# Optimization experiments

Hardware: AMD Instinct MI355X
Metric: run time of the kernel (lower is better)

The kernel has to match this reference:

```python
import jax, jax.numpy as jnp
import numpy as np

B, D, SL, N, H, LL = 2, 128, 1024, 64, 4, 4
LN_EPS = 1e-5
DIST_EPS = 1e-8


def _ln(x, g, b):
    m = x.mean(-1, keepdims=True)
    v = ((x - m) ** 2).mean(-1, keepdims=True)
    return (x - m) / jnp.sqrt(v + LN_EPS) * g + b


def _sla(x, qw, qb, kw, kb, vw, vb, ow, ob):
    # x: [B, R, C, D]; rank-1 scaled linear attention (head_qk_dim = 1)
    Bq, R, C, Dd = x.shape
    Hh = qw.shape[0]
    hd = Dd // Hh
    q = jnp.einsum('brcd,hd->brhc', x, qw) + qb[:, None]   # [B,R,H,C]
    k = jnp.einsum('brcd,hd->brhc', x, kw) + kb[:, None]
    q = jax.nn.elu(q) + 1.0
    k = jax.nn.elu(k) + 1.0
    q = q / q.mean(-1, keepdims=True)
    k = k / k.sum(-1, keepdims=True)
    v = (jnp.einsum('brcd,ed->brce', x, vw) + vb).reshape(Bq, R, C, Hh, hd)
    v = v.transpose(0, 1, 3, 2, 4)                         # [B,R,H,C,hd]
    ktv = jnp.einsum('brhc,brhce->brhe', k, v)             # [B,R,H,hd]
    V = jnp.einsum('brhc,brhe->brche', q, ktv)             # [B,R,C,H,hd]
    V = V.reshape(Bq, R, C, Dd)
    return jnp.einsum('brcd,ed->brce', V, ow) + ob


def _forward(x, rq_w, rq_b, rk_w, rk_b, rv_w, rv_b, ro_w, ro_b,
             cq_w, cq_b, ck_w, ck_b, cv_w, cv_b, co_w, co_b,
             ln_r_g, ln_r_b, ln_c_g, ln_c_b, ln_f_g, ln_f_b,
             f1_w, f1_b, f2_w, f2_b):
    y = x.transpose(0, 2, 3, 1)   # [B, L, N, D] channels-last

    def layer(y, p):
        (rqw, rqb, rkw, rkb, rvw, rvb, row_, rob,
         cqw, cqb, ckw, ckb, cvw, cvb, cow, cob,
         lrg, lrb, lcg, lcb, lfg, lfb, f1w, f1b, f2w, f2b) = p
        # row attention: rows = L, cols = N
        y = y + _sla(_ln(y, lrg, lrb), rqw, rqb, rkw, rkb, rvw, rvb, row_, rob)
        # col attention: rows = N, cols = L
        hc = _ln(y, lcg, lcb).swapaxes(1, 2)
        y = y + _sla(hc, cqw, cqb, ckw, ckb, cvw, cvb, cow, cob).swapaxes(1, 2)
        # FFN (1x1 convs == pointwise linears)
        hf = _ln(y, lfg, lfb)
        hf = jax.nn.gelu(jnp.einsum('blnd,ed->blne', hf, f1w) + f1b, approximate=False)
        y = y + (jnp.einsum('blne,de->blnd', hf, f2w) + f2b)
        return y, None

    params = (rq_w, rq_b, rk_w, rk_b, rv_w, rv_b, ro_w, ro_b,
              cq_w, cq_b, ck_w, ck_b, cv_w, cv_b, co_w, co_b,
              ln_r_g, ln_r_b, ln_c_g, ln_c_b, ln_f_g, ln_f_b,
              f1_w, f1_b, f2_w, f2_b)
    y, _ = jax.lax.scan(layer, y, params)

    # Euclidean pairwise distance head (use_cls=False): mean over sites 1..L
    xb = y[:, 1:].mean(axis=1)                 # [B, N, D]
    i0, i1 = np.tril_indices(N, -1)            # lower=True, diff=True ordering
    diffs = xb[:, i0] - xb[:, i1]              # [B, n_pairs, D]
    return jnp.sqrt(jnp.sum(diffs * diffs, axis=-1) + DIST_EPS)


def setup_inputs() -> dict:
    key = jax.random.key(0)
    ks = jax.random.split(key, 12)
    s = 0.02
    z = lambda *sh: jnp.zeros(sh, jnp.float32)
    o = lambda *sh: jnp.ones(sh, jnp.float32)
    w = lambda k, sh: jax.random.normal(k, sh, jnp.float32) * s
    p = {'x': jax.random.normal(ks[0], (B, D, SL, N), jnp.float32)}
    p['rq_w'] = w(ks[1], (LL, H, D)); p['rq_b'] = z(LL, H)
    p['rk_w'] = w(ks[2], (LL, H, D)); p['rk_b'] = z(LL, H)
    p['rv_w'] = w(ks[3], (LL, D, D)); p['rv_b'] = z(LL, D)
    p['ro_w'] = w(ks[4], (LL, D, D)); p['ro_b'] = z(LL, D)
    p['cq_w'] = w(ks[5], (LL, H, D)); p['cq_b'] = z(LL, H)
    p['ck_w'] = w(ks[6], (LL, H, D)); p['ck_b'] = z(LL, H)
    p['cv_w'] = w(ks[7], (LL, D, D)); p['cv_b'] = z(LL, D)
    p['co_w'] = w(ks[8], (LL, D, D)); p['co_b'] = z(LL, D)
    p['ln_r_g'] = o(LL, D); p['ln_r_b'] = z(LL, D)
    p['ln_c_g'] = o(LL, D); p['ln_c_b'] = z(LL, D)
    p['ln_f_g'] = o(LL, D); p['ln_f_b'] = z(LL, D)
    p['f1_w'] = w(ks[9], (LL, 4 * D, D)); p['f1_b'] = z(LL, 4 * D)
    p['f2_w'] = w(ks[10], (LL, D, 4 * D)); p['f2_b'] = z(LL, D)
    return p


def reference(x, rq_w, rq_b, rk_w, rk_b, rv_w, rv_b, ro_w, ro_b,
              cq_w, cq_b, ck_w, ck_b, cv_w, cv_b, co_w, co_b,
              ln_r_g, ln_r_b, ln_c_g, ln_c_b, ln_f_g, ln_f_b,
              f1_w, f1_b, f2_w, f2_b):
    return _forward(x, rq_w, rq_b, rk_w, rk_b, rv_w, rv_b, ro_w, ro_b,
                    cq_w, cq_b, ck_w, ck_b, cv_w, cv_b, co_w, co_b,
                    ln_r_g, ln_r_b, ln_c_g, ln_c_b, ln_f_g, ln_f_b,
                    f1_w, f1_b, f2_w, f2_b)
```

## Files before the change

### kernel.cpp

```cpp
#include <hip/hip_runtime.h>
#include <math.h>

#define LCNT 4

typedef float f32x4 __attribute__((ext_vector_type(4)));
typedef short bf16x8 __attribute__((ext_vector_type(8)));
typedef unsigned int u32;

__device__ __forceinline__ ushort bfr(float x){
  unsigned int b = __float_as_uint(x);
  return (ushort)((b + 0x7FFFu + ((b>>16)&1u)) >> 16);
}
__device__ __forceinline__ unsigned int pk2(float a, float b){
  return (unsigned int)bfr(a) | ((unsigned int)bfr(b)<<16);
}
__device__ __forceinline__ float bflo(u32 u){ return __uint_as_float(u<<16); }
__device__ __forceinline__ float bfhi(u32 u){ return __uint_as_float(u & 0xffff0000u); }
__device__ __forceinline__ float fast_gelu(float v){
  float v2 = v*v;
  float u = v*(-1.5957691f - 0.0713548162f*v2);
  float e = __expf(u);
  return v*__builtin_amdgcn_rcpf(1.f + e);
}
__device__ __forceinline__ void gl_lds16(const void* g, void* l){
  __builtin_amdgcn_global_load_lds(
      (const __attribute__((address_space(1))) u32*)g,
      (__attribute__((address_space(3))) u32*)l, 16, 0, 0);
}

__global__ __launch_bounds__(256) void k_transpose(const float* __restrict__ x,
                                                   float* __restrict__ y){
  int g = blockIdx.x;
  int b = g >> 10, l = g & 1023;
  __shared__ float sh[128*65];
  for (int idx = threadIdx.x; idx < 128*64; idx += 256){
    int d = idx >> 6, n = idx & 63;
    sh[d*65+n] = x[(((size_t)b*128 + d)*1024 + l)*64 + n];
  }
  __syncthreads();
  for (int idx = threadIdx.x; idx < 128*64; idx += 256){
    int n = idx >> 7, d = idx & 127;
    y[((size_t)g*64 + n)*128 + d] = sh[d*65+n];
  }
}

__global__ __launch_bounds__(256) void k_cvt(const float* __restrict__ src,
                                             ushort* __restrict__ dst, int n4){
  int i = blockIdx.x*256 + threadIdx.x;
  if (i < n4){
    float4 v = ((const float4*)src)[i];
    ushort4 p; p.x=bfr(v.x); p.y=bfr(v.y); p.z=bfr(v.z); p.w=bfr(v.w);
    ((ushort4*)dst)[i] = p;
  }
}

#define HSTRB 136
__global__ __launch_bounds__(256) void k_row(
    float* __restrict__ y,
    const float* __restrict__ rqw, const float* __restrict__ rqb,
    const float* __restrict__ rkw, const float* __restrict__ rkb,
    const float* __restrict__ rvw, const float* __restrict__ rvb,
    const float* __restrict__ roW, const float* __restrict__ rob,
    const float* __restrict__ lrg, const float* __restrict__ lrb,
    const float* __restrict__ cqw, const float* __restrict__ cqb,
    const float* __restrict__ ckw, const float* __restrict__ ckb,
    const float* __restrict__ lcg, const float* __restrict__ lcb,
    float2* __restrict__ stats,
    float* __restrict__ qout, float* __restrict__ kout)
{
  int g = blockIdx.x;
  __shared__ __align__(16) ushort sh_h[64*HSTRB];
  __shared__ __align__(16) float sh_w4[2048];
  __shared__ float sh_q[256], sh_k[256];
  __shared__ __align__(16) float sh_hkP[512];
  __shared__ __align__(16) float sh_ktv[128];
  int tid = threadIdx.x;
  int wid = tid>>6, ln = tid&63;

  {
    const float* wsrc = (wid==0)?rqw:(wid==1)?rkw:(wid==2)?cqw:ckw;
    gl_lds16(wsrc + ln*4,       &sh_w4[wid*512]);
    gl_lds16(wsrc + 256 + ln*4, &sh_w4[wid*512 + 256]);
  }

  int ttk = tid>>2, s4 = tid&3;
  float* yr = y + ((size_t)g*64 + ttk)*128 + s4*32;
  float4 v[8];
  #pragma unroll
  for (int i=0;i<8;i++) v[i] = *(const float4*)(yr + i*4);
  float sum = 0.f;
  #pragma unroll
  for (int i=0;i<8;i++) sum += v[i].x+v[i].y+v[i].z+v[i].w;
  sum += __shfl_xor(sum,1); sum += __shfl_xor(sum,2);
  float mean = sum*(1.0f/128.0f);
  float vs = 0.f;
  #pragma unroll
  for (int i=0;i<8;i++){
    v[i].x-=mean; v[i].y-=mean; v[i].z-=mean; v[i].w-=mean;
    vs += v[i].x*v[i].x+v[i].y*v[i].y+v[i].z*v[i].z+v[i].w*v[i].w;
  }
  vs += __shfl_xor(vs,1); vs += __shfl_xor(vs,2);
  float rstd = rsqrtf(vs*(1.0f/128.0f) + 1e-5f);
  {
    const float* gp = lrg + s4*32; const float* bp = lrb + s4*32;
    ushort* hrow = &sh_h[ttk*HSTRB + s4*32];
    #pragma unroll
    for (int i=0;i<8;i++){
      float4 g4 = *(const float4*)(gp+i*4);
      float4 b4 = *(const float4*)(bp+i*4);
      uint2 o2;
      o2.x = pk2(v[i].x*rstd*g4.x+b4.x, v[i].y*rstd*g4.y+b4.y);
      o2.y = pk2(v[i].z*rstd*g4.z+b4.z, v[i].w*rstd*g4.w+b4.w);
      *(uint2*)&hrow[i*4] = o2;
    }
  }
  __syncthreads();

  int h = tid>>6, n = tid&63;
  {
    float qr = rqb[h], kr = rkb[h];
    const int4* hp = (const int4*)&sh_h[n*HSTRB];
    const float4* qwp = (const float4*)&sh_w4[h*128];
    const float4* kwp = (const float4*)&sh_w4[512 + h*128];
    #pragma unroll 4
    for (int j=0;j<16;j++){
      int4 h8 = hp[j];
      float4 qa = qwp[2*j], qb4 = qwp[2*j+1];
      float4 ka = kwp[2*j], kb4 = kwp[2*j+1];
      float h0=bflo((u32)h8.x), h1=bfhi((u32)h8.x);
      float h2=bflo((u32)h8.y), h3=bfhi((u32)h8.y);
      float h4=bflo((u32)h8.z), h5=bfhi((u32)h8.z);
      float h6=bflo((u32)h8.w), h7=bfhi((u32)h8.w);
      qr += h0*qa.x+h1*qa.y+h2*qa.z+h3*qa.w + h4*qb4.x+h5*qb4.y+h6*qb4.z+h7*qb4.w;
      kr += h0*ka.x+h1*ka.y+h2*ka.z+h3*ka.w + h4*kb4.x+h5*kb4.y+h6*kb4.z+h7*kb4.w;
    }
    qr = qr > 0.f ? qr + 1.f : __expf(qr);
    kr = kr > 0.f ? kr + 1.f : __expf(kr);
    float qs = qr; for (int m=32;m>=1;m>>=1) qs += __shfl_xor(qs, m);
    float ks = kr; for (int m=32;m>=1;m>>=1) ks += __shfl_xor(ks, m);
    sh_q[h*64+n] = qr * (64.f/qs);
    sh_k[h*64+n] = kr * (1.f/ks);
  }
  __syncthreads();
  #pragma unroll
  for (int r=0;r<2;r++){
    int idx = tid + r*256;
    int hh = idx>>7, d = idx&127;
    float acc = 0.f;
    #pragma unroll 4
    for (int nn=0;nn<64;nn++)
      acc += sh_k[hh*64+nn]*bflo((u32)sh_h[nn*HSTRB+d]);
    sh_hkP[hh*128+d] = acc;
  }
  __syncthreads();
  if (tid < 128){
    float acc = rvb[tid];
    const float4* vr = (const float4*)(rvw + (size_t)tid*128);
    const float4* hp2 = (const float4*)(sh_hkP + (tid>>5)*128);
    #pragma unroll 8
    for (int j=0;j<32;j++){
      float4 a = vr[j], bq = hp2[j];
      acc += a.x*bq.x + a.y*bq.y + a.z*bq.z + a.w*bq.w;
    }
    sh_ktv[tid] = acc;
  }
  __syncthreads();
  #pragma unroll
  for (int r=0;r<2;r++){
    int idx = tid + r*256;
    int hh = idx>>7, e = idx&127;
    float acc = 0.f;
    const float4* orow = (const float4*)(roW + (size_t)e*128 + hh*32);
    const float4* kt = (const float4*)(sh_ktv + hh*32);
    #pragma unroll
    for (int j=0;j<8;j++){
      float4 a = orow[j], bq = kt[j];
      acc += a.x*bq.x + a.y*bq.y + a.z*bq.z + a.w*bq.w;
    }
    sh_hkP[hh*128+e] = acc;
  }
  __syncthreads();
  {
    float q0=sh_q[ttk], q1=sh_q[64+ttk], q2=sh_q[128+ttk], q3=sh_q[192+ttk];
    const float4* P4 = (const float4*)sh_hkP;
    #pragma unroll
    for (int i=0;i<8;i++){
      int d4 = s4*8 + i;
      float4 p0=P4[d4], p1=P4[32+d4], p2=P4[64+d4], p3=P4[96+d4];
      float4 o4=*(const float4*)&rob[s4*32+i*4];
      v[i].x += mean + o4.x + q0*p0.x+q1*p1.x+q2*p2.x+q3*p3.x;
      v[i].y += mean + o4.y + q0*p0.y+q1*p1.y+q2*p2.y+q3*p3.y;
      v[i].z += mean + o4.z + q0*p0.z+q1*p1.z+q2*p2.z+q3*p3.z;
      v[i].w += mean + o4.w + q0*p0.w+q1*p1.w+q2*p2.w+q3*p3.w;
      *(float4*)(yr + i*4) = v[i];
    }
  }
  float sum2 = 0.f;
  #pragma unroll
  for (int i=0;i<8;i++) sum2 += v[i].x+v[i].y+v[i].z+v[i].w;
  sum2 += __shfl_xor(sum2,1); sum2 += __shfl_xor(sum2,2);
  float cmean = sum2*(1.0f/128.0f);
  float cvs = 0.f;
  #pragma unroll
  for (int i=0;i<8;i++){
    v[i].x-=cmean; v[i].y-=cmean; v[i].z-=cmean; v[i].w-=cmean;
    cvs += v[i].x*v[i].x+v[i].y*v[i].y+v[i].z*v[i].z+v[i].w*v[i].w;
  }
  cvs += __shfl_xor(cvs,1); cvs += __shfl_xor(cvs,2);
  float crstd = rsqrtf(cvs*(1.0f/128.0f) + 1e-5f);
  if (s4 == 0) stats[(size_t)g*64 + ttk] = make_float2(cmean, crstd);
  {
    const float* gp = lcg + s4*32; const float* bp = lcb + s4*32;
    ushort* hrow = &sh_h[ttk*HSTRB + s4*32];
    #pragma unroll
    for (int i=0;i<8;i++){
      float4 g4 = *(const float4*)(gp+i*4);
      float4 b4 = *(const float4*)(bp+i*4);
      uint2 o2;
      o2.x = pk2(v[i].x*crstd*g4.x+b4.x, v[i].y*crstd*g4.y+b4.y);
      o2.y = pk2(v[i].z*crstd*g4.z+b4.z, v[i].w*crstd*g4.w+b4.w);
      *(uint2*)&hrow[i*4] = o2;
    }
  }
  __syncthreads();
  {
    float qv = cqb[h], kv = ckb[h];
    const int4* hp = (const int4*)&sh_h[n*HSTRB];
    const float4* qwp = (const float4*)&sh_w4[1024 + h*128];
    const float4* kwp = (const float4*)&sh_w4[1536 + h*128];
    #pragma unroll 4
    for (int j=0;j<16;j++){
      int4 h8 = hp[j];
      float4 qa = qwp[2*j], qb4 = qwp[2*j+1];
      float4 ka = kwp[2*j], kb4 = kwp[2*j+1];
      float h0=bflo((u32)h8.x), h1=bfhi((u32)h8.x);
      float h2=bflo((u32)h8.y), h3=bfhi((u32)h8.y);
      float h4=bflo((u32)h8.z), h5=bfhi((u32)h8.z);
      float h6=bflo((u32)h8.w), h7=bfhi((u32)h8.w);
      qv += h0*qa.x+h1*qa.y+h2*qa.z+h3*qa.w + h4*qb4.x+h5*qb4.y+h6*qb4.z+h7*qb4.w;
      kv += h0*ka.x+h1*ka.y+h2*ka.z+h3*ka.w + h4*kb4.x+h5*kb4.y+h6*kb4.z+h7*kb4.w;
    }
    qv = qv > 0.f ? qv + 1.f : __expf(qv);
    kv = kv > 0.f ? kv + 1.f : __expf(kv);
    size_t o = (size_t)g*256 + tid;
    qout[o] = qv; kout[o] = kv;
  }
}

__global__ __launch_bounds__(256) void k_qsum(const float* __restrict__ qin,
                                              float* __restrict__ qsp){
  int gg = blockIdx.x;
  int c = gg&7, b = gg>>3;
  int tid = threadIdx.x;
  const float* qp = qin + ((size_t)b*1024 + c*128)*256 + tid;
  float s = 0.f;
  #pragma unroll 4
  for (int j=0;j<128;j++){ s += *qp; qp += 256; }
  qsp[(size_t)gg*256 + tid] = s;
}

__global__ __launch_bounds__(256) void k_col_s1(
    const float* __restrict__ y, const float2* __restrict__ stats,
    const float* __restrict__ kin,
    float* __restrict__ s1p, float* __restrict__ Ab, float* __restrict__ Bb)
{
  int gg = blockIdx.x;
  int s = gg & 7, n = (gg>>3) & 63, b = gg>>9;
  int tid = threadIdx.x;
  int li = tid>>7, d = tid&127;
  const float* kp = kin + (size_t)b*262144 + n;
  float a0=0.f,a1=0.f,a2=0.f,a3=0.f;
  float A0=0.f,A1=0.f,A2=0.f,A3=0.f;
  float B0=0.f,B1=0.f,B2=0.f,B3=0.f;
  for (int j=0;j<64;j++){
    int l = s*128 + 2*j + li;
    size_t t = ((size_t)(b*1024+l)*64+n);
    float2 st = stats[t];
    float w = st.y * y[t*128 + d];
    float rm = st.y*st.x;
    const float* kl = kp + (size_t)l*256;
    float k0 = kl[0], k1 = kl[64], k2 = kl[128], k3 = kl[192];
    a0 += k0*w; a1 += k1*w; a2 += k2*w; a3 += k3*w;
    A0 += k0; A1 += k1; A2 += k2; A3 += k3;
    B0 += k0*rm; B1 += k1*rm; B2 += k2*rm; B3 += k3*rm;
  }
  __shared__ float shr[512];
  __shared__ float sAB[8];
  if (li == 1){
    shr[0*128+d]=a0; shr[1*128+d]=a1; shr[2*128+d]=a2; shr[3*128+d]=a3;
    if (d==0){ sAB[0]=A0; sAB[1]=A1; sAB[2]=A2; sAB[3]=A3;
               sAB[4]=B0; sAB[5]=B1; sAB[6]=B2; sAB[7]=B3; }
  }
  __syncthreads();
  if (li == 0){
    float* out = s1p + (size_t)gg*512;
    out[0*128+d] = a0 + shr[0*128+d];
    out[1*128+d] = a1 + shr[1*128+d];
    out[2*128+d] = a2 + shr[2*128+d];
    out[3*128+d] = a3 + shr[3*128+d];
    if (d==0){
      Ab[gg*4+0]=A0+sAB[0]; Ab[gg*4+1]=A1+sAB[1];
      Ab[gg*4+2]=A2+sAB[2]; Ab[gg*4+3]=A3+sAB[3];
      Bb[gg*4+0]=B0+sAB[4]; Bb[gg*4+1]=B1+sAB[5];
      Bb[gg*4+2]=B2+sAB[6]; Bb[gg*4+3]=B3+sAB[7];
    }
  }
}

__global__ __launch_bounds__(256) void k_col_ktvP(
    const float* __restrict__ s1p,
    const float* __restrict__ Ab, const float* __restrict__ Bb,
    const float* __restrict__ qsp,
    const float* __restrict__ vw, const float* __restrict__ vb,
    const float* __restrict__ ow,
    const float* __restrict__ lcg, const float* __restrict__ lcb,
    float* __restrict__ Pout)
{
  int gg = blockIdx.x;
  int b = gg>>6, n = gg&63;
  __shared__ float sh_hk[512];
  __shared__ float sh_ktv[128];
  __shared__ float sh_A[4], sh_B[4], sh_qs[4];
  int tid = threadIdx.x;
  #pragma unroll
  for (int r = 0; r < 2; r++){
    int idx = tid + r*256;
    float acc = 0.f;
    #pragma unroll
    for (int s = 0; s < 8; s++) acc += s1p[((size_t)gg*8 + s)*512 + idx];
    sh_hk[idx] = acc;
  }
  if (tid < 4){
    float a=0.f, bb=0.f, q=0.f;
    #pragma unroll
    for (int s = 0; s < 8; s++){ a += Ab[(gg*8+s)*4+tid]; bb += Bb[(gg*8+s)*4+tid]; }
    #pragma unroll
    for (int c = 0; c < 8; c++) q += qsp[((b*8+c)<<8) + (tid<<6) + n];
    sh_A[tid]=a; sh_B[tid]=bb; sh_qs[tid] = 1024.f/q;
  }
  __syncthreads();
  #pragma unroll
  for (int r = 0; r < 2; r++){
    int idx = tid + r*256;
    int h = idx>>7, d = idx&127;
    sh_hk[idx] = lcg[d]*((sh_hk[idx]-sh_B[h])/sh_A[h]) + lcb[d];
  }
  __syncthreads();
  if (tid < 128){
    float acc = vb[tid];
    const float* vr = vw + (size_t)tid*128;
    const float* hp2 = sh_hk + (tid>>5)*128;
    #pragma unroll 4
    for (int d = 0; d < 128; d++) acc += vr[d]*hp2[d];
    sh_ktv[tid] = acc;
  }
  __syncthreads();
  #pragma unroll
  for (int r = 0; r < 2; r++){
    int idx = tid + r*256;
    int hh = idx >> 7, e = idx & 127;
    float acc = 0.f;
    const float* orow = ow + (size_t)e*128 + hh*32;
    #pragma unroll 4
    for (int j = 0; j < 32; j++) acc += orow[j]*sh_ktv[hh*32+j];
    Pout[(size_t)gg*512 + hh*128 + e] = acc * sh_qs[hh];
  }
}

__global__ __launch_bounds__(512, 4) void k_ffn(
    float* __restrict__ y,
    const float* __restrict__ qbuf, const float* __restrict__ Pb,
    const float* __restrict__ cob,
    const float* __restrict__ gam, const float* __restrict__ bet,
    const ushort* __restrict__ w1b, const float* __restrict__ b1,
    const ushort* __restrict__ w2b, const float* __restrict__ b2)
{
  __shared__ __align__(16) ushort pool[29952];
  ushort* sW1 = pool;
  ushort* sW2 = pool + 8192;
  ushort* sH  = pool + 16384;
  ushort* sHf = pool + 25088;
  float*  sF  = (float*)pool;
  int tid = threadIdx.x;
  int g = blockIdx.x;
  size_t tb = (size_t)g*64;

  int wid = tid>>6, ln = tid&63;
  int lr = ln&15, gq = ln>>4;
  int wt = wid>>1, we = wid&1;
  int t0 = wt*16;

  #pragma unroll
  for (int i = 0; i < 2; i++){
    int row = wid*8 + i*4 + (ln>>4);
    gl_lds16(w1b + (size_t)row*128 + (((ln&15) ^ (row&7))<<3),
             &sW1[(wid*8 + i*4)*128]);
  }
  #pragma unroll
  for (int i = 0; i < 2; i++){
    int row = wid*16 + i*8 + (ln>>3);
    gl_lds16(w2b + (size_t)row*512 + (((ln&7) ^ (row&7))<<3),
             &sW2[(wid*16 + i*8)*64]);
  }

  int ttk = tid>>3, s8 = tid&7;
  float* yr = y + (tb+ttk)*128 + s8*16;
  float4 v[4];
  float fmean;
  {
    #pragma unroll
    for (int i = 0; i < 4; i++) v[i] = *(const float4*)(yr + i*4);
    const float* qp = qbuf + (size_t)g*256 + ttk;
    float q0 = qp[0], q1 = qp[64], q2 = qp[128], q3 = qp[192];
    const float* pr = Pb + ((size_t)((g>>10)*64 + ttk))*512 + s8*16;
    #pragma unroll
    for (int i = 0; i < 4; i++){
      float4 p0 = *(const float4*)(pr + i*4);
      float4 p1 = *(const float4*)(pr + 128 + i*4);
      float4 p2 = *(const float4*)(pr + 256 + i*4);
      float4 p3 = *(const float4*)(pr + 384 + i*4);
      float4 c4 = *(const float4*)&cob[s8*16 + i*4];
      v[i].x += c4.x + q0*p0.x+q1*p1.x+q2*p2.x+q3*p3.x;
      v[i].y += c4.y + q0*p0.y+q1*p1.y+q2*p2.y+q3*p3.y;
      v[i].z += c4.z + q0*p0.z+q1*p1.z+q2*p2.z+q3*p3.z;
      v[i].w += c4.w + q0*p0.w+q1*p1.w+q2*p2.w+q3*p3.w;
    }
    float sum = 0.f;
    #pragma unroll
    for (int i = 0; i < 4; i++) sum += v[i].x+v[i].y+v[i].z+v[i].w;
    sum += __shfl_xor(sum,1); sum += __shfl_xor(sum,2); sum += __shfl_xor(sum,4);
    fmean = sum*(1.0f/128.0f);
    float vs = 0.f;
    #pragma unroll
    for (int i = 0; i < 4; i++){
      v[i].x-=fmean; v[i].y-=fmean; v[i].z-=fmean; v[i].w-=fmean;
      vs += v[i].x*v[i].x+v[i].y*v[i].y+v[i].z*v[i].z+v[i].w*v[i].w;
    }
    vs += __shfl_xor(vs,1); vs += __shfl_xor(vs,2); vs += __shfl_xor(vs,4);
    float rstd = rsqrtf(vs*(1.0f/128.0f) + 1e-5f);
    const float* gp = gam + s8*16; const float* bp = bet + s8*16;
    #pragma unroll
    for (int i = 0; i < 2; i++){
      float4 ga = *(const float4*)(gp + i*8),     gb = *(const float4*)(gp + i*8 + 4);
      float4 ba = *(const float4*)(bp + i*8),     bb = *(const float4*)(bp + i*8 + 4);
      float4 va = v[i*2], vb2 = v[i*2+1];
      int4 o;
      o.x = (int)pk2(va.x*rstd*ga.x+ba.x,  va.y*rstd*ga.y+ba.y);
      o.y = (int)pk2(va.z*rstd*ga.z+ba.z,  va.w*rstd*ga.w+ba.w);
      o.z = (int)pk2(vb2.x*rstd*gb.x+bb.x, vb2.y*rstd*gb.y+bb.y);
      o.w = (int)pk2(vb2.z*rstd*gb.z+bb.z, vb2.w*rstd*gb.w+bb.w);
      *(int4*)&sH[ttk*136 + s8*16 + i*8] = o;
    }
  }
  __syncthreads();

  f32x4 acc2[4] = {};

  for (int c = 0; c < 8; c++){
    f32x4 acc1[2] = {};
    #pragma unroll
    for (int ks = 0; ks < 4; ks++){
      bf16x8 bfv = *(const bf16x8*)&sH[(t0+lr)*136 + ks*32 + gq*8];
      #pragma unroll
      for (int i = 0; i < 2; i++){
        int er = we*32 + i*16 + lr;
        bf16x8 afv = *(const bf16x8*)&sW1[er*128 + ((((ks<<2)|gq) ^ (lr&7))<<3)];
        acc1[i] = __builtin_amdgcn_mfma_f32_16x16x32_bf16(afv, bfv, acc1[i], 0, 0, 0);
      }
    }
    #pragma unroll
    for (int i = 0; i < 2; i++){
      float4 bb = *(const float4*)&b1[c*64 + we*32 + i*16 + gq*4];
      ushort4 pk;
      pk.x = bfr(fast_gelu(acc1[i][0] + bb.x));
      pk.y = bfr(fast_gelu(acc1[i][1] + bb.y));
      pk.z = bfr(fast_gelu(acc1[i][2] + bb.z));
      pk.w = bfr(fast_gelu(acc1[i][3] + bb.w));
      *(ushort4*)&sHf[(t0+lr)*72 + we*32 + i*16 + gq*4] = pk;
    }
    __syncthreads();
    if (c < 7){
      #pragma unroll
      for (int i = 0; i < 2; i++){
        int row = wid*8 + i*4 + (ln>>4);
        gl_lds16(w1b + (size_t)(c+1)*8192 + (size_t)row*128 + (((ln&15) ^ (row&7))<<3),
                 &sW1[(wid*8 + i*4)*128]);
      }
    }
    #pragma unroll
    for (int ks = 0; ks < 2; ks++){
      bf16x8 bfv = *(const bf16x8*)&sHf[(t0+lr)*72 + ks*32 + gq*8];
      #pragma unroll
      for (int j = 0; j < 4; j++){
        int dr = we*64 + j*16 + lr;
        bf16x8 afv = *(const bf16x8*)&sW2[dr*64 + ((((ks<<2)|gq) ^ (lr&7))<<3)];
        acc2[j] = __builtin_amdgcn_mfma_f32_16x16x32_bf16(afv, bfv, acc2[j], 0, 0, 0);
      }
    }
    __syncthreads();
    if (c < 7){
      #pragma unroll
      for (int i = 0; i < 2; i++){
        int row = wid*16 + i*8 + (ln>>3);
        gl_lds16(w2b + (size_t)row*512 + (c+1)*64 + (((ln&7) ^ (row&7))<<3),
                 &sW2[(wid*16 + i*8)*64]);
      }
    }
  }

  #pragma unroll
  for (int j = 0; j < 4; j++){
    float4 fo; fo.x=acc2[j][0]; fo.y=acc2[j][1]; fo.z=acc2[j][2]; fo.w=acc2[j][3];
    *(float4*)&sF[(t0+lr)*132 + we*64 + j*16 + gq*4] = fo;
  }
  __syncthreads();
  #pragma unroll
  for (int i = 0; i < 4; i++){
    float4 f = *(const float4*)&sF[ttk*132 + s8*16 + i*4];
    float4 b4 = *(const float4*)&b2[s8*16 + i*4];
    float4 o;
    o.x = v[i].x + fmean + f.x + b4.x;
    o.y = v[i].y + fmean + f.y + b4.y;
    o.z = v[i].z + fmean + f.z + b4.z;
    o.w = v[i].w + fmean + f.w + b4.w;
    *(float4*)(yr + i*4) = o;
  }
}

__global__ __launch_bounds__(128) void k_xbp(const float* __restrict__ y,
                                             float* __restrict__ xbq){
  int gg = blockIdx.x;
  int s = gg & 3, n = (gg>>2) & 63, b = gg>>8;
  int d = threadIdx.x;
  float acc = 0.f;
  int l0 = s*256 + (s==0 ? 1 : 0);
  const float* p = y + (((size_t)b*1024 + l0)*64 + n)*128 + d;
  for (int l = l0; l < s*256+256; l++){ acc += *p; p += 64*128; }
  xbq[(size_t)gg*128 + d] = acc;
}
__global__ __launch_bounds__(128) void k_xbr(const float* __restrict__ xbq,
                                             float* __restrict__ xb){
  int gg = blockIdx.x;
  int d = threadIdx.x;
  const float* q = xbq + (size_t)gg*512;
  xb[(size_t)gg*128 + d] = (q[d] + q[128+d] + q[256+d] + q[384+d]) * (1.0f/1023.0f);
}

__global__ __launch_bounds__(64) void k_dist(const float* __restrict__ xb,
                                             float* __restrict__ out){
  int p = blockIdx.x;
  int b = p >= 2016 ? 1 : 0;
  int pr = p - b*2016;
  int i0 = (int)((1.0f + sqrtf(1.0f + 8.0f*(float)pr))*0.5f);
  while (i0*(i0-1)/2 > pr) i0--;
  while ((i0+1)*i0/2 <= pr) i0++;
  int i1 = pr - i0*(i0-1)/2;
  int lane = threadIdx.x;
  const float* xa = xb + ((size_t)b*64 + i0)*128;
  const float* xc = xb + ((size_t)b*64 + i1)*128;
  float d0 = xa[lane]-xc[lane], d1 = xa[lane+64]-xc[lane+64];
  float s = d0*d0 + d1*d1;
  for (int m=32;m>=1;m>>=1) s += __shfl_xor(s, m);
  if (lane == 0) out[p] = sqrtf(s + 1e-8f);
}

extern "C" void kernel_launch(void* const* d_in, const int* in_sizes, int n_in,
                              void* d_out, int out_size, void* d_ws, size_t ws_size,
                              hipStream_t stream){
  const float* x    = (const float*)d_in[0];
  const float* rq_w = (const float*)d_in[1];  const float* rq_b = (const float*)d_in[2];
  const float* rk_w = (const float*)d_in[3];  const float* rk_b = (const float*)d_in[4];
  const float* rv_w = (const float*)d_in[5];  const float* rv_b = (const float*)d_in[6];
  const float* ro_w = (const float*)d_in[7];  const float* ro_b = (const float*)d_in[8];
  const float* cq_w = (const float*)d_in[9];  const float* cq_b = (const float*)d_in[10];
  const float* ck_w = (const float*)d_in[11]; const float* ck_b = (const float*)d_in[12];
  const float* cv_w = (const float*)d_in[13]; const float* cv_b = (const float*)d_in[14];
  const float* co_w = (const float*)d_in[15]; const float* co_b = (const float*)d_in[16];
  const float* lrg  = (const float*)d_in[17]; const float* lrb  = (const float*)d_in[18];
  const float* lcg  = (const float*)d_in[19]; const float* lcb  = (const float*)d_in[20];
  const float* lfg  = (const float*)d_in[21]; const float* lfb  = (const float*)d_in[22];
  const float* f1w  = (const float*)d_in[23]; const float* f1b  = (const float*)d_in[24];
  const float* f2w  = (const float*)d_in[25]; const float* f2b  = (const float*)d_in[26];

  float* ws = (float*)d_ws;
  float*  y   = ws;
  float2* st  = (float2*)(ws + 16777216);
  float*  qb_ = ws + 17039360;
  float*  kb_ = ws + 17563648;
  float*  Pb  = ws + 18087936;
  float*  s1p = ws + 19136512;
  float*  xb  = ws + 19661824;
  ushort* w1b = (ushort*)(ws + 19678208);
  ushort* w2b = (ushort*)(ws + 19809280);
  float*  xbq = ws + 19940352;
  float*  Ab  = ws + 20005888;
  float*  Bb  = ws + 20009984;
  float*  qsp = ws + 20014080;

  k_transpose<<<dim3(2048), dim3(256), 0, stream>>>(x, y);
  k_cvt<<<dim3(256), dim3(256), 0, stream>>>(f1w, w1b, 65536);
  k_cvt<<<dim3(256), dim3(256), 0, stream>>>(f2w, w2b, 65536);
  for (int l = 0; l < LCNT; l++){
    k_row<<<dim3(2048), dim3(256), 0, stream>>>(y,
        rq_w + l*512, rq_b + l*4, rk_w + l*512, rk_b + l*4,
        rv_w + (size_t)l*16384, rv_b + l*128, ro_w + (size_t)l*16384, ro_b + l*128,
        lrg + l*128, lrb + l*128,
        cq_w + l*512, cq_b + l*4, ck_w + l*512, ck_b + l*4,
        lcg + l*128, lcb + l*128,
        st, qb_, kb_);
    k_qsum<<<dim3(16), dim3(256), 0, stream>>>(qb_, qsp);
    k_col_s1<<<dim3(1024), dim3(256), 0, stream>>>(y, st, kb_, s1p, Ab, Bb);
    k_col_ktvP<<<dim3(128), dim3(256), 0, stream>>>(s1p, Ab, Bb, qsp,
        cv_w + (size_t)l*16384, cv_b + l*128, co_w + (size_t)l*16384,
        lcg + l*128, lcb + l*128, Pb);
    k_ffn<<<dim3(2048), dim3(512), 0, stream>>>(y, qb_, Pb, co_b + l*128,
        lfg + l*128, lfb + l*128,
        w1b + (size_t)l*65536, f1b + l*512, w2b + (size_t)l*65536, f2b + l*128);
  }
  k_xbp<<<dim3(512), dim3(128), 0, stream>>>(y, xbq);
  k_xbr<<<dim3(128), dim3(128), 0, stream>>>(xbq, xb);
  k_dist<<<dim3(4032), dim3(64), 0, stream>>>(xb, (float*)d_out);
}
```

Before: 1.049 ms.

## Fuse FFN with next layer's row attention into one kernel

Adds a combined kernel that runs the FFN of layer l and then, on the same 64-token tile still held in registers and LDS, the row attention and column-LN/q/k projection of layer l+1. Only the first layer's row pass stays a separate launch. This removes one kernel launch per layer and one full read/write of y between the FFN and row passes. In exchange the fused kernel is longer, uses more registers, reuses the LDS pool across phases, and k_ffn's launch bounds drop from 4 to 2 blocks per SM, which may lower occupancy.

```diff
diff --git a/kernel.cpp b/kernel.cpp
--- a/kernel.cpp
+++ b/kernel.cpp
@@ -76,13 +76,11 @@
   __shared__ __align__(16) float sh_ktv[128];
   int tid = threadIdx.x;
   int wid = tid>>6, ln = tid&63;
-
   {
     const float* wsrc = (wid==0)?rqw:(wid==1)?rkw:(wid==2)?cqw:ckw;
     gl_lds16(wsrc + ln*4,       &sh_w4[wid*512]);
     gl_lds16(wsrc + 256 + ln*4, &sh_w4[wid*512 + 256]);
   }
-
   int ttk = tid>>2, s4 = tid&3;
   float* yr = y + ((size_t)g*64 + ttk)*128 + s4*32;
   float4 v[8];
@@ -115,7 +113,6 @@
     }
   }
   __syncthreads();
-
   int h = tid>>6, n = tid&63;
   {
     float qr = rqb[h], kr = rkb[h];
@@ -367,7 +364,7 @@
   }
 }
 
-__global__ __launch_bounds__(512, 4) void k_ffn(
+__global__ __launch_bounds__(512, 2) void k_ffn(
     float* __restrict__ y,
     const float* __restrict__ qbuf, const float* __restrict__ Pb,
     const float* __restrict__ cob,
@@ -524,6 +521,348 @@
     o.z = v[i].z + fmean + f.z + b4.z;
     o.w = v[i].w + fmean + f.w + b4.w;
     *(float4*)(yr + i*4) = o;
+  }
+}
+
+__global__ __launch_bounds__(512, 2) void k_fr(
+    float* __restrict__ y,
+    const float* __restrict__ qbuf, const float* __restrict__ Pb,
+    const float* __restrict__ cob,
+    const float* __restrict__ fgam, const float* __restrict__ fbet,
+    const ushort* __restrict__ w1b, const float* __restrict__ b1,
+    const ushort* __restrict__ w2b, const float* __restrict__ b2,
+    const float* __restrict__ rqw, const float* __restrict__ rqb,
+    const float* __restrict__ rkw, const float* __restrict__ rkb,
+    const float* __restrict__ rvb_, const float* __restrict__ rvw,
+    const float* __restrict__ roW, const float* __restrict__ rob,
+    const float* __restrict__ lrg, const float* __restrict__ lrb,
+    const float* __restrict__ cqw, const float* __restrict__ cqb,
+    const float* __restrict__ ckw, const float* __restrict__ ckb,
+    const float* __restrict__ lcg, const float* __restrict__ lcb,
+    float2* __restrict__ stats,
+    float* __restrict__ qout, float* __restrict__ kout)
+{
+  __shared__ __align__(16) ushort pool[29952];
+  ushort* sW1 = pool;
+  ushort* sW2 = pool + 8192;
+  ushort* sH  = pool + 16384;
+  ushort* sHf = pool + 25088;
+  float*  sF  = (float*)pool;
+  ushort* rh   = pool;
+  float*  rw4  = (float*)(pool + 8704);
+  float*  rQ   = (float*)(pool + 12800);
+  float*  rK   = (float*)(pool + 13312);
+  float*  rhkP = (float*)(pool + 13824);
+  float*  rktv = (float*)(pool + 14848);
+  int tid = threadIdx.x;
+  int g = blockIdx.x;
+  size_t tb = (size_t)g*64;
+
+  int wid = tid>>6, ln = tid&63;
+  int lr = ln&15, gq = ln>>4;
+  int wt = wid>>1, we = wid&1;
+  int t0 = wt*16;
+
+  #pragma unroll
+  for (int i = 0; i < 2; i++){
+    int row = wid*8 + i*4 + (ln>>4);
+    gl_lds16(w1b + (size_t)row*128 + (((ln&15) ^ (row&7))<<3),
+             &sW1[(wid*8 + i*4)*128]);
+  }
+  #pragma unroll
+  for (int i = 0; i < 2; i++){
+    int row = wid*16 + i*8 + (ln>>3);
+    gl_lds16(w2b + (size_t)row*512 + (((ln&7) ^ (row&7))<<3),
+             &sW2[(wid*16 + i*8)*64]);
+  }
+
+  int ttk = tid>>3, s8 = tid&7;
+  float* yr = y + (tb+ttk)*128 + s8*16;
+  float4 v[4];
+  float fmean;
+  {
+    #pragma unroll
+    for (int i = 0; i < 4; i++) v[i] = *(const float4*)(yr + i*4);
+    const float* qp = qbuf + (size_t)g*256 + ttk;
+    float q0 = qp[0], q1 = qp[64], q2 = qp[128], q3 = qp[192];
+    const float* pr = Pb + ((size_t)((g>>10)*64 + ttk))*512 + s8*16;
+    #pragma unroll
+    for (int i = 0; i < 4; i++){
+      float4 p0 = *(const float4*)(pr + i*4);
+      float4 p1 = *(const float4*)(pr + 128 + i*4);
+      float4 p2 = *(const float4*)(pr + 256 + i*4);
+      float4 p3 = *(const float4*)(pr + 384 + i*4);
+      float4 c4 = *(const float4*)&cob[s8*16 + i*4];
+      v[i].x += c4.x + q0*p0.x+q1*p1.x+q2*p2.x+q3*p3.x;
+      v[i].y += c4.y + q0*p0.y+q1*p1.y+q2*p2.y+q3*p3.y;
+      v[i].z += c4.z + q0*p0.z+q1*p1.z+q2*p2.z+q3*p3.z;
+      v[i].w += c4.w + q0*p0.w+q1*p1.w+q2*p2.w+q3*p3.w;
+    }
+    float sum = 0.f;
+    #pragma unroll
+    for (int i = 0; i < 4; i++) sum += v[i].x+v[i].y+v[i].z+v[i].w;
+    sum += __shfl_xor(sum,1); sum += __shfl_xor(sum,2); sum += __shfl_xor(sum,4);
+    fmean = sum*(1.0f/128.0f);
+    float vs = 0.f;
+    #pragma unroll
+    for (int i = 0; i < 4; i++){
+      v[i].x-=fmean; v[i].y-=fmean; v[i].z-=fmean; v[i].w-=fmean;
+      vs += v[i].x*v[i].x+v[i].y*v[i].y+v[i].z*v[i].z+v[i].w*v[i].w;
+    }
+    vs += __shfl_xor(vs,1); vs += __shfl_xor(vs,2); vs += __shfl_xor(vs,4);
+    float rstd = rsqrtf(vs*(1.0f/128.0f) + 1e-5f);
+    const float* gp = fgam + s8*16; const float* bp = fbet + s8*16;
+    #pragma unroll
+    for (int i = 0; i < 2; i++){
+      float4 ga = *(const float4*)(gp + i*8),     gb = *(const float4*)(gp + i*8 + 4);
+      float4 ba = *(const float4*)(bp + i*8),     bb = *(const float4*)(bp + i*8 + 4);
+      float4 va = v[i*2], vb2 = v[i*2+1];
+      int4 o;
+      o.x = (int)pk2(va.x*rstd*ga.x+ba.x,  va.y*rstd*ga.y+ba.y);
+      o.y = (int)pk2(va.z*rstd*ga.z+ba.z,  va.w*rstd*ga.w+ba.w);
+      o.z = (int)pk2(vb2.x*rstd*gb.x+bb.x, vb2.y*rstd*gb.y+bb.y);
+      o.w = (int)pk2(vb2.z*rstd*gb.z+bb.z, vb2.w*rstd*gb.w+bb.w);
+      *(int4*)&sH[ttk*136 + s8*16 + i*8] = o;
+    }
+  }
+  __syncthreads();
+
+  f32x4 acc2[4] = {};
+  for (int c = 0; c < 8; c++){
+    f32x4 acc1[2] = {};
+    #pragma unroll
+    for (int ks = 0; ks < 4; ks++){
+      bf16x8 bfv = *(const bf16x8*)&sH[(t0+lr)*136 + ks*32 + gq*8];
+      #pragma unroll
+      for (int i = 0; i < 2; i++){
+        int er = we*32 + i*16 + lr;
+        bf16x8 afv = *(const bf16x8*)&sW1[er*128 + ((((ks<<2)|gq) ^ (lr&7))<<3)];
+        acc1[i] = __builtin_amdgcn_mfma_f32_16x16x32_bf16(afv, bfv, acc1[i], 0, 0, 0);
+      }
+    }
+    #pragma unroll
+    for (int i = 0; i < 2; i++){
+      float4 bb = *(const float4*)&b1[c*64 + we*32 + i*16 + gq*4];
+      ushort4 pk;
+      pk.x = bfr(fast_gelu(acc1[i][0] + bb.x));
+      pk.y = bfr(fast_gelu(acc1[i][1] + bb.y));
+      pk.z = bfr(fast_gelu(acc1[i][2] + bb.z));
+      pk.w = bfr(fast_gelu(acc1[i][3] + bb.w));
+      *(ushort4*)&sHf[(t0+lr)*72 + we*32 + i*16 + gq*4] = pk;
+    }
+    __syncthreads();
+    if (c < 7){
+      #pragma unroll
+      for (int i = 0; i < 2; i++){
+        int row = wid*8 + i*4 + (ln>>4);
+        gl_lds16(w1b + (size_t)(c+1)*8192 + (size_t)row*128 + (((ln&15) ^ (row&7))<<3),
+                 &sW1[(wid*8 + i*4)*128]);
+      }
+    }
+    #pragma unroll
+    for (int ks = 0; ks < 2; ks++){
+      bf16x8 bfv = *(const bf16x8*)&sHf[(t0+lr)*72 + ks*32 + gq*8];
+      #pragma unroll
+      for (int j = 0; j < 4; j++){
+        int dr = we*64 + j*16 + lr;
+        bf16x8 afv = *(const bf16x8*)&sW2[dr*64 + ((((ks<<2)|gq) ^ (lr&7))<<3)];
+        acc2[j] = __builtin_amdgcn_mfma_f32_16x16x32_bf16(afv, bfv, acc2[j], 0, 0, 0);
+      }
+    }
+    __syncthreads();
+    if (c < 7){
+      #pragma unroll
+      for (int i = 0; i < 2; i++){
+        int row = wid*16 + i*8 + (ln>>3);
+        gl_lds16(w2b + (size_t)row*512 + (c+1)*64 + (((ln&7) ^ (row&7))<<3),
+                 &sW2[(wid*16 + i*8)*64]);
+      }
+    }
+  }
+
+  #pragma unroll
+  for (int j = 0; j < 4; j++){
+    float4 fo; fo.x=acc2[j][0]; fo.y=acc2[j][1]; fo.z=acc2[j][2]; fo.w=acc2[j][3];
+    *(float4*)&sF[(t0+lr)*132 + we*64 + j*16 + gq*4] = fo;
+  }
+  __syncthreads();
+  #pragma unroll
+  for (int i = 0; i < 4; i++){
+    float4 f = *(const float4*)&sF[ttk*132 + s8*16 + i*4];
+    float4 b4 = *(const float4*)&b2[s8*16 + i*4];
+    v[i].x += fmean + f.x + b4.x;
+    v[i].y += fmean + f.y + b4.y;
+    v[i].z += fmean + f.z + b4.z;
+    v[i].w += fmean + f.w + b4.w;
+  }
+  __syncthreads();
+
+  {
+    const float* wsrc = (wid<2)?rqw:(wid<4)?rkw:(wid<6)?cqw:ckw;
+    gl_lds16(wsrc + (wid&1)*256 + ln*4, &rw4[(size_t)wid*256]);
+  }
+
+  float rmean;
+  {
+    float sum = 0.f;
+    #pragma unroll
+    for (int i = 0; i < 4; i++) sum += v[i].x+v[i].y+v[i].z+v[i].w;
+    sum += __shfl_xor(sum,1); sum += __shfl_xor(sum,2); sum += __shfl_xor(sum,4);
+    rmean = sum*(1.0f/128.0f);
+    float vs = 0.f;
+    #pragma unroll
+    for (int i = 0; i < 4; i++){
+      v[i].x-=rmean; v[i].y-=rmean; v[i].z-=rmean; v[i].w-=rmean;
+      vs += v[i].x*v[i].x+v[i].y*v[i].y+v[i].z*v[i].z+v[i].w*v[i].w;
+    }
+    vs += __shfl_xor(vs,1); vs += __shfl_xor(vs,2); vs += __shfl_xor(vs,4);
+    float rstd = rsqrtf(vs*(1.0f/128.0f) + 1e-5f);
+    const float* gp = lrg + s8*16; const float* bp = lrb + s8*16;
+    ushort* hrow = &rh[ttk*HSTRB + s8*16];
+    #pragma unroll
+    for (int i = 0; i < 2; i++){
+      float4 ga = *(const float4*)(gp + i*8),  gb = *(const float4*)(gp + i*8 + 4);
+      float4 ba = *(const float4*)(bp + i*8),  bb = *(const float4*)(bp + i*8 + 4);
+      float4 va = v[i*2], vb2 = v[i*2+1];
+      int4 o;
+      o.x = (int)pk2(va.x*rstd*ga.x+ba.x,  va.y*rstd*ga.y+ba.y);
+      o.y = (int)pk2(va.z*rstd*ga.z+ba.z,  va.w*rstd*ga.w+ba.w);
+      o.z = (int)pk2(vb2.x*rstd*gb.x+bb.x, vb2.y*rstd*gb.y+bb.y);
+      o.w = (int)pk2(vb2.z*rstd*gb.z+bb.z, vb2.w*rstd*gb.w+bb.w);
+      *(int4*)&hrow[i*8] = o;
+    }
+  }
+  __syncthreads();
+
+  if (tid < 256){
+    int h = tid>>6, n = tid&63;
+    float qr = rqb[h], kr = rkb[h];
+    const int4* hp = (const int4*)&rh[n*HSTRB];
+    const float4* qwp = (const float4*)&rw4[h*128];
+    const float4* kwp = (const float4*)&rw4[512 + h*128];
+    #pragma unroll 4
+    for (int j=0;j<16;j++){
+      int4 h8 = hp[j];
+      float4 qa = qwp[2*j], qb4 = qwp[2*j+1];
+      float4 ka = kwp[2*j], kb4 = kwp[2*j+1];
+      float h0=bflo((u32)h8.x), h1=bfhi((u32)h8.x);
+      float h2=bflo((u32)h8.y), h3=bfhi((u32)h8.y);
+      float h4=bflo((u32)h8.z), h5=bfhi((u32)h8.z);
+      float h6=bflo((u32)h8.w), h7=bfhi((u32)h8.w);
+      qr += h0*qa.x+h1*qa.y+h2*qa.z+h3*qa.w + h4*qb4.x+h5*qb4.y+h6*qb4.z+h7*qb4.w;
+      kr += h0*ka.x+h1*ka.y+h2*ka.z+h3*ka.w + h4*kb4.x+h5*kb4.y+h6*kb4.z+h7*kb4.w;
+    }
+    qr = qr > 0.f ? qr + 1.f : __expf(qr);
+    kr = kr > 0.f ? kr + 1.f : __expf(kr);
+    float qs = qr; for (int m=32;m>=1;m>>=1) qs += __shfl_xor(qs, m);
+    float ks = kr; for (int m=32;m>=1;m>>=1) ks += __shfl_xor(ks, m);
+    rQ[h*64+n] = qr * (64.f/qs);
+    rK[h*64+n] = kr * (1.f/ks);
+  }
+  __syncthreads();
+  {
+    int hh = tid>>7, d = tid&127;
+    float acc = 0.f;
+    #pragma unroll 4
+    for (int nn=0;nn<64;nn++)
+      acc += rK[hh*64+nn]*bflo((u32)rh[nn*HSTRB+d]);
+    rhkP[hh*128+d] = acc;
+  }
+  __syncthreads();
+  if (tid < 128){
+    float acc = rvb_[tid];
+    const float4* vr = (const float4*)(rvw + (size_t)tid*128);
+    const float4* hp2 = (const float4*)(rhkP + (tid>>5)*128);
+    #pragma unroll 8
+    for (int j=0;j<32;j++){
+      float4 a = vr[j], bq = hp2[j];
+      acc += a.x*bq.x + a.y*bq.y + a.z*bq.z + a.w*bq.w;
+    }
+    rktv[tid] = acc;
+  }
+  __syncthreads();
+  {
+    int hh = tid>>7, e = tid&127;
+    float acc = 0.f;
+    const float4* orow = (const float4*)(roW + (size_t)e*128 + hh*32);
+    const float4* kt = (const float4*)(rktv + hh*32);
+    #pragma unroll
+    for (int j=0;j<8;j++){
+      float4 a = orow[j], bq = kt[j];
+      acc += a.x*bq.x + a.y*bq.y + a.z*bq.z + a.w*bq.w;
+    }
+    rhkP[hh*128+e] = acc;
+  }
+  __syncthreads();
+  {
+    float q0=rQ[ttk], q1=rQ[64+ttk], q2=rQ[128+ttk], q3=rQ[192+ttk];
+    #pragma unroll
+    for (int i=0;i<4;i++){
+      float4 p0 = *(const float4*)&rhkP[s8*16 + i*4];
+      float4 p1 = *(const float4*)&rhkP[128 + s8*16 + i*4];
+      float4 p2 = *(const float4*)&rhkP[256 + s8*16 + i*4];
+      float4 p3 = *(const float4*)&rhkP[384 + s8*16 + i*4];
+      float4 o4 = *(const float4*)&rob[s8*16 + i*4];
+      v[i].x += rmean + o4.x + q0*p0.x+q1*p1.x+q2*p2.x+q3*p3.x;
+      v[i].y += rmean + o4.y + q0*p0.y+q1*p1.y+q2*p2.y+q3*p3.y;
+      v[i].z += rmean + o4.z + q0*p0.z+q1*p1.z+q2*p2.z+q3*p3.z;
+      v[i].w += rmean + o4.w + q0*p0.w+q1*p1.w+q2*p2.w+q3*p3.w;
+      *(float4*)(yr + i*4) = v[i];
+    }
+  }
+  {
+    float sum2 = 0.f;
+    #pragma unroll
+    for (int i=0;i<4;i++) sum2 += v[i].x+v[i].y+v[i].z+v[i].w;
+    sum2 += __shfl_xor(sum2,1); sum2 += __shfl_xor(sum2,2); sum2 += __shfl_xor(sum2,4);
+    float cmean = sum2*(1.0f/128.0f);
+    float cvs = 0.f;
+    #pragma unroll
+    for (int i=0;i<4;i++){
+      v[i].x-=cmean; v[i].y-=cmean; v[i].z-=cmean; v[i].w-=cmean;
+      cvs += v[i].x*v[i].x+v[i].y*v[i].y+v[i].z*v[i].z+v[i].w*v[i].w;
+    }
+    cvs += __shfl_xor(cvs,1); cvs += __shfl_xor(cvs,2); cvs += __shfl_xor(cvs,4);
+    float crstd = rsqrtf(cvs*(1.0f/128.0f) + 1e-5f);
+    if (s8 == 0) stats[(size_t)g*64 + ttk] = make_float2(cmean, crstd);
+    const float* gp = lcg + s8*16; const float* bp = lcb + s8*16;
+    ushort* hrow = &rh[ttk*HSTRB + s8*16];
+    #pragma unroll
+    for (int i = 0; i < 2; i++){
+      float4 ga = *(const float4*)(gp + i*8),  gb = *(const float4*)(gp + i*8 + 4);
+      float4 ba = *(const float4*)(bp + i*8),  bb = *(const float4*)(bp + i*8 + 4);
+      float4 va = v[i*2], vb2 = v[i*2+1];
+      int4 o;
+      o.x = (int)pk2(va.x*crstd*ga.x+ba.x,  va.y*crstd*ga.y+ba.y);
+      o.y = (int)pk2(va.z*crstd*ga.z+ba.z,  va.w*crstd*ga.w+ba.w);
+      o.z = (int)pk2(vb2.x*crstd*gb.x+bb.x, vb2.y*crstd*gb.y+bb.y);
+      o.w = (int)pk2(vb2.z*crstd*gb.z+bb.z, vb2.w*crstd*gb.w+bb.w);
+      *(int4*)&hrow[i*8] = o;
+    }
+  }
+  __syncthreads();
+  if (tid < 256){
+    int h = tid>>6, n = tid&63;
+    float qv = cqb[h], kv = ckb[h];
+    const int4* hp = (const int4*)&rh[n*HSTRB];
+    const float4* qwp = (const float4*)&rw4[1024 + h*128];
+    const float4* kwp = (const float4*)&rw4[1536 + h*128];
+    #pragma unroll 4
+    for (int j=0;j<16;j++){
+      int4 h8 = hp[j];
+      float4 qa = qwp[2*j], qb4 = qwp[2*j+1];
+      float4 ka = kwp[2*j], kb4 = kwp[2*j+1];
+      float h0=bflo((u32)h8.x), h1=bfhi((u32)h8.x);
+      float h2=bflo((u32)h8.y), h3=bfhi((u32)h8.y);
+      float h4=bflo((u32)h8.z), h5=bfhi((u32)h8.z);
+      float h6=bflo((u32)h8.w), h7=bfhi((u32)h8.w);
+      qv += h0*qa.x+h1*qa.y+h2*qa.z+h3*qa.w + h4*qb4.x+h5*qb4.y+h6*qb4.z+h7*qb4.w;
+      kv += h0*ka.x+h1*ka.y+h2*ka.z+h3*ka.w + h4*kb4.x+h5*kb4.y+h6*kb4.z+h7*kb4.w;
+    }
+    qv = qv > 0.f ? qv + 1.f : __expf(qv);
+    kv = kv > 0.f ? kv + 1.f : __expf(kv);
+    size_t o = (size_t)g*256 + tid;
+    qout[o] = qv; kout[o] = kv;
   }
 }
 
@@ -600,22 +939,33 @@
   k_transpose<<<dim3(2048), dim3(256), 0, stream>>>(x, y);
   k_cvt<<<dim3(256), dim3(256), 0, stream>>>(f1w, w1b, 65536);
   k_cvt<<<dim3(256), dim3(256), 0, stream>>>(f2w, w2b, 65536);
+  k_row<<<dim3(2048), dim3(256), 0, stream>>>(y,
+      rq_w, rq_b, rk_w, rk_b, rv_w, rv_b, ro_w, ro_b,
+      lrg, lrb, cq_w, cq_b, ck_w, ck_b, lcg, lcb,
+      st, qb_, kb_);
   for (int l = 0; l < LCNT; l++){
-    k_row<<<dim3(2048), dim3(256), 0, stream>>>(y,
-        rq_w + l*512, rq_b + l*4, rk_w + l*512, rk_b + l*4,
-        rv_w + (size_t)l*16384, rv_b + l*128, ro_w + (size_t)l*16384, ro_b + l*128,
-        lrg + l*128, lrb + l*128,
-        cq_w + l*512, cq_b + l*4, ck_w + l*512, ck_b + l*4,
-        lcg + l*128, lcb + l*128,
-        st, qb_, kb_);
     k_qsum<<<dim3(16), dim3(256), 0, stream>>>(qb_, qsp);
     k_col_s1<<<dim3(1024), dim3(256), 0, stream>>>(y, st, kb_, s1p, Ab, Bb);
     k_col_ktvP<<<dim3(128), dim3(256), 0, stream>>>(s1p, Ab, Bb, qsp,
         cv_w + (size_t)l*16384, cv_b + l*128, co_w + (size_t)l*16384,
         lcg + l*128, lcb + l*128, Pb);
-    k_ffn<<<dim3(2048), dim3(512), 0, stream>>>(y, qb_, Pb, co_b + l*128,
-        lfg + l*128, lfb + l*128,
-        w1b + (size_t)l*65536, f1b + l*512, w2b + (size_t)l*65536, f2b + l*128);
+    if (l < LCNT-1){
+      int m = l+1;
+      k_fr<<<dim3(2048), dim3(512), 0, stream>>>(y, qb_, Pb, co_b + l*128,
+          lfg + l*128, lfb + l*128,
+          w1b + (size_t)l*65536, f1b + l*512, w2b + (size_t)l*65536, f2b + l*128,
+          rq_w + m*512, rq_b + m*4, rk_w + m*512, rk_b + m*4,
+          rv_b + m*128, rv_w + (size_t)m*16384,
+          ro_w + (size_t)m*16384, ro_b + m*128,
+          lrg + m*128, lrb + m*128,
+          cq_w + m*512, cq_b + m*4, ck_w + m*512, ck_b + m*4,
+          lcg + m*128, lcb + m*128,
+          st, qb_, kb_);
+    } else {
+      k_ffn<<<dim3(2048), dim3(512), 0, stream>>>(y, qb_, Pb, co_b + l*128,
+          lfg + l*128, lfb + l*128,
+          w1b + (size_t)l*65536, f1b + l*512, w2b + (size_t)l*65536, f2b + l*128);
+    }
   }
   k_xbp<<<dim3(512), dim3(128), 0, stream>>>(y, xbq);
   k_xbr<<<dim3(128), dim3(128), 0, stream>>>(xbq, xb);
```

Measured after the change: 1.072 ms. +2.2%, slower.
